# Optimization experiments

Measured on AMD Instinct MI355X. Metric: run time of the kernel, lower is better.

Reference implementation:

```python
import jax, jax.numpy as jnp
import numpy as np

N_USERS = 50000
N_ITEMS = 4000
BATCH = 256
EPS = 1e-8


def setup_inputs() -> dict:
    key = jax.random.key(0)
    k1, k2 = jax.random.split(key)
    explicit_feedback = jax.random.uniform(k1, (N_USERS, N_ITEMS), dtype=jnp.float32)
    user_ids = jax.random.randint(k2, (BATCH,), 0, N_USERS, dtype=jnp.int64)
    return {"explicit_feedback": explicit_feedback, "user_ids": user_ids, "num_neighbors": 10}


def reference(explicit_feedback, user_ids, num_neighbors):
    F = explicit_feedback                              # [U, I]
    # norm = row-wise SUM OF SQUARES (no sqrt), as in the original module
    norm_all = jnp.maximum(jnp.sum(F * F, axis=1), EPS)          # [U]
    users = F[user_ids]                                          # [B, I]
    norm_users = jnp.maximum(jnp.sum(users * users, axis=1), EPS)  # [B]
    sim = (users @ F.T) / norm_users[:, None] / norm_all[None, :]  # [B, U]
    neighbor_sim, neighbor_idx = jax.lax.top_k(sim, num_neighbors)  # [B, k]
    weights = neighbor_sim / jnp.sum(neighbor_sim, axis=1, keepdims=True)  # [B, k]
    neighbors = F[neighbor_idx]                                   # [B, k, I]
    ratings = jnp.einsum("bk,bki->bi", weights, neighbors)        # [B, I]
    return ratings
```

## Files before the change

kernel.cpp:

```cpp
#include <hip/hip_runtime.h>
#include <hip/hip_bf16.h>

#define N_USERS 50000
#define N_ITEMS 4000
#define BATCH   256
#define KSTEPS  125
#define NWG     391
#define NEG_INF (-3.402823466e38f)

typedef __attribute__((ext_vector_type(8)))  __bf16 bfrag;
typedef __attribute__((ext_vector_type(16))) float  f32x16;

__device__ __forceinline__ unsigned short f2bf(float f) {
  unsigned u = __float_as_uint(f);
  return (unsigned short)((u + 0x7FFFu + ((u >> 16) & 1u)) >> 16);
}

__global__ __launch_bounds__(256) void prep_pack(
    const float* __restrict__ F, const int* __restrict__ uids,
    unsigned short* __restrict__ apack) {
  int m = blockIdx.x;
  size_t base = (size_t)uids[m] * N_ITEMS;
  for (int kk = threadIdx.x * 4; kk < N_ITEMS; kk += 1024) {
    float4 v = *(const float4*)(F + base + kk);
    ushort4 o;
    o.x = f2bf(v.x); o.y = f2bf(v.y); o.z = f2bf(v.z); o.w = f2bf(v.w);
    *(ushort4*)(apack + (size_t)(kk >> 5) * 8192 + m * 32 + (kk & 31)) = o;
  }
}

__global__ __launch_bounds__(256, 2) void gemm_topk(
    const float* __restrict__ F, const unsigned short* __restrict__ apack,
    float2* __restrict__ wstop) {
  union Smem {
    struct { unsigned short As[256][40]; unsigned short Bs[128][40]; } g;
    float dump[4][64][33];
  };
  __shared__ Smem sm;
  __shared__ float norms[128];

  const int tid  = threadIdx.x;
  const int w    = tid >> 6, lane = tid & 63;
  const int lrow = lane & 31, lhalf = lane >> 5;
  const int n0   = blockIdx.x * 128;

  const uint4* aptr = (const uint4*)apack + tid * 4;
  const int brow = tid >> 1, bh = tid & 1;
  const bool bvalid = (n0 + brow) < N_USERS;
  const float4* bptr = (const float4*)(F + (size_t)(bvalid ? (n0 + brow) : 0) * N_ITEMS) + bh * 4;

  f32x16 acc[2][4];
  #pragma unroll
  for (int i = 0; i < 2; ++i)
    #pragma unroll
    for (int j = 0; j < 4; ++j)
      #pragma unroll
      for (int e = 0; e < 16; ++e) acc[i][j][e] = 0.f;

  float ssq = 0.f;
  uint4 ar[4]; float4 br[4];

  {
    ar[0] = aptr[0]; ar[1] = aptr[1]; ar[2] = aptr[2]; ar[3] = aptr[3];
    if (bvalid) { br[0] = bptr[0]; br[1] = bptr[1]; br[2] = bptr[2]; br[3] = bptr[3]; }
    else { br[0] = br[1] = br[2] = br[3] = make_float4(0.f, 0.f, 0.f, 0.f); }
  }

  for (int ks = 0; ks < KSTEPS; ++ks) {
    if (ks) __syncthreads();
    uint4* adst = (uint4*)&sm.g.As[tid][0];
    adst[0] = ar[0]; adst[1] = ar[1]; adst[2] = ar[2]; adst[3] = ar[3];
    {
      const float* vv = (const float*)br;
      union { unsigned short s[8]; uint4 v; } h0, h1;
      #pragma unroll
      for (int e = 0; e < 8; ++e) h0.s[e] = f2bf(vv[e]);
      #pragma unroll
      for (int e = 0; e < 8; ++e) h1.s[e] = f2bf(vv[8 + e]);
      #pragma unroll
      for (int e = 0; e < 16; ++e) ssq = fmaf(vv[e], vv[e], ssq);
      *(uint4*)&sm.g.Bs[brow][bh * 16]     = h0.v;
      *(uint4*)&sm.g.Bs[brow][bh * 16 + 8] = h1.v;
    }
    __syncthreads();
    if (ks + 1 < KSTEPS) {
      const uint4* ap = aptr + (ks + 1) * 1024;
      ar[0] = ap[0]; ar[1] = ap[1]; ar[2] = ap[2]; ar[3] = ap[3];
      if (bvalid) {
        const float4* bp = bptr + (ks + 1) * 8;
        br[0] = bp[0]; br[1] = bp[1]; br[2] = bp[2]; br[3] = bp[3];
      }
    }
    #pragma unroll
    for (int s = 0; s < 2; ++s) {
      bfrag af[2], bfr[4];
      #pragma unroll
      for (int i = 0; i < 2; ++i)
        af[i] = *(const bfrag*)&sm.g.As[(2 * w + i) * 32 + lrow][s * 16 + lhalf * 8];
      #pragma unroll
      for (int j = 0; j < 4; ++j)
        bfr[j] = *(const bfrag*)&sm.g.Bs[j * 32 + lrow][s * 16 + lhalf * 8];
      #pragma unroll
      for (int i = 0; i < 2; ++i)
        #pragma unroll
        for (int j = 0; j < 4; ++j)
          acc[i][j] = __builtin_amdgcn_mfma_f32_32x32x16_bf16(af[i], bfr[j], acc[i][j], 0, 0, 0);
    }
  }

  ssq += __shfl_xor(ssq, 1);
  if (bh == 0) norms[brow] = fmaxf(ssq, 1e-8f);

  float tv[8]; int ti[8];
  #pragma unroll
  for (int q = 0; q < 8; ++q) { tv[q] = NEG_INF; ti[q] = 0; }

  #pragma unroll
  for (int p = 0; p < 4; ++p) {
    __syncthreads();
    {
      const int   ugc = n0 + 32 * p + lrow;
      const float inv = 1.0f / norms[32 * p + lrow];
      #pragma unroll
      for (int i = 0; i < 2; ++i)
        #pragma unroll
        for (int r = 0; r < 16; ++r) {
          int mrow = 32 * i + (r & 3) + 8 * (r >> 2) + 4 * lhalf;
          float v = (ugc < N_USERS) ? acc[i][p][r] * inv : NEG_INF;
          sm.dump[w][mrow][lrow] = v;
        }
    }
    __syncthreads();
    for (int c = 0; c < 32; ++c) {
      float v = sm.dump[w][lane][c];
      int ci = n0 + 32 * p + c;
      #pragma unroll
      for (int q = 0; q < 8; ++q) {
        bool gt = v > tv[q];
        float ov = tv[q]; int oi = ti[q];
        tv[q] = gt ? v : ov; ti[q] = gt ? ci : oi;
        v = gt ? ov : v;     ci = gt ? oi : ci;
      }
    }
  }

  float2* dst = wstop + ((size_t)blockIdx.x * 256 + tid) * 8;
  #pragma unroll
  for (int q = 0; q < 8; ++q) dst[q] = make_float2(tv[q], __int_as_float(ti[q]));
}

__global__ __launch_bounds__(64) void merge_topk(
    const float2* __restrict__ wstop, int* __restrict__ cand) {
  const int b = blockIdx.x, l = threadIdx.x;
  float tv[8]; int ti[8];
  #pragma unroll
  for (int q = 0; q < 8; ++q) { tv[q] = NEG_INF; ti[q] = 0; }
  for (int c = l; c < NWG * 8; c += 64) {
    int wg = c >> 3, q = c & 7;
    float2 e = wstop[((size_t)wg * 256 + b) * 8 + q];
    float v = e.x; int ci = __float_as_int(e.y);
    #pragma unroll
    for (int q2 = 0; q2 < 8; ++q2) {
      bool gt = v > tv[q2];
      float ov = tv[q2]; int oi = ti[q2];
      tv[q2] = gt ? v : ov; ti[q2] = gt ? ci : oi;
      v = gt ? ov : v;      ci = gt ? oi : ci;
    }
  }
  __shared__ float sv[512];
  __shared__ int   si[512];
  #pragma unroll
  for (int q = 0; q < 8; ++q) { sv[l * 8 + q] = tv[q]; si[l * 8 + q] = ti[q]; }
  __syncthreads();
  if (l == 0) {
    float bv[32]; int bi[32];
    #pragma unroll
    for (int q = 0; q < 32; ++q) { bv[q] = NEG_INF; bi[q] = 0; }
    for (int n = 0; n < 512; ++n) {
      float v = sv[n];
      if (v > bv[31]) {
        int ci = si[n];
        #pragma unroll
        for (int q = 0; q < 32; ++q) {
          bool gt = v > bv[q];
          float ov = bv[q]; int oi = bi[q];
          bv[q] = gt ? v : ov; bi[q] = gt ? ci : oi;
          v = gt ? ov : v;     ci = gt ? oi : ci;
        }
      }
    }
    #pragma unroll
    for (int q = 0; q < 32; ++q) cand[b * 32 + q] = bi[q];
  }
}

__global__ __launch_bounds__(64) void rescore(
    const float* __restrict__ F, const int* __restrict__ uids,
    const int* __restrict__ cand, double* __restrict__ simx) {
  const int pr = blockIdx.x;
  const int b  = pr >> 5;
  const int ci = cand[pr];
  const float* fa = F + (size_t)uids[b] * N_ITEMS;
  const float* fc = F + (size_t)ci * N_ITEMS;
  double dot = 0.0, ss = 0.0;
  for (int k = threadIdx.x * 4; k < N_ITEMS; k += 256) {
    float4 a = *(const float4*)(fa + k);
    float4 c = *(const float4*)(fc + k);
    dot += (double)a.x * c.x + (double)a.y * c.y + (double)a.z * c.z + (double)a.w * c.w;
    ss  += (double)c.x * c.x + (double)c.y * c.y + (double)c.z * c.z + (double)c.w * c.w;
  }
  #pragma unroll
  for (int off = 32; off > 0; off >>= 1) {
    dot += __shfl_down(dot, off);
    ss  += __shfl_down(ss, off);
  }
  if (threadIdx.x == 0) simx[pr] = dot / fmax(ss, 1e-8);
}

__global__ __launch_bounds__(256) void finalize(
    const float* __restrict__ F, const int* __restrict__ cand,
    const double* __restrict__ simx, float* __restrict__ out) {
  const int b = blockIdx.x;
  __shared__ float wsh[10];
  __shared__ int   ish[10];
  if (threadIdx.x == 0) {
    double bv[10]; int bi[10];
    #pragma unroll
    for (int q = 0; q < 10; ++q) { bv[q] = -1.0e300; bi[q] = 0; }
    for (int n = 0; n < 32; ++n) {
      double v = simx[b * 32 + n];
      int ci = cand[b * 32 + n];
      #pragma unroll
      for (int q = 0; q < 10; ++q) {
        bool gt = v > bv[q];
        double ov = bv[q]; int oi = bi[q];
        bv[q] = gt ? v : ov; bi[q] = gt ? ci : oi;
        v = gt ? ov : v;     ci = gt ? oi : ci;
      }
    }
    double s = 0.0;
    #pragma unroll
    for (int q = 0; q < 10; ++q) s += bv[q];
    #pragma unroll
    for (int q = 0; q < 10; ++q) { wsh[q] = (float)(bv[q] / s); ish[q] = bi[q]; }
  }
  __syncthreads();
  float wr[10]; size_t ro[10];
  #pragma unroll
  for (int q = 0; q < 10; ++q) { wr[q] = wsh[q]; ro[q] = (size_t)ish[q] * N_ITEMS; }
  for (int i = threadIdx.x; i < N_ITEMS; i += 256) {
    float a = 0.f;
    #pragma unroll
    for (int q = 0; q < 10; ++q) a = fmaf(wr[q], F[ro[q] + i], a);
    out[b * N_ITEMS + i] = a;
  }
}

extern "C" void kernel_launch(void* const* d_in, const int* in_sizes, int n_in,
                              void* d_out, int out_size, void* d_ws, size_t ws_size,
                              hipStream_t stream) {
  const float* F    = (const float*)d_in[0];
  const int*   uids = (const int*)d_in[1];
  float* out = (float*)d_out;
  char*  ws  = (char*)d_ws;

  unsigned short* apack = (unsigned short*)ws;
  float2* wstop = (float2*)(ws + 2097152);
  int*    cand  = (int*)(ws + 2097152 + 6406144);
  double* simx  = (double*)(ws + 2097152 + 6406144 + 32768);

  prep_pack<<<dim3(BATCH), dim3(256), 0, stream>>>(F, uids, apack);
  gemm_topk<<<dim3(NWG),   dim3(256), 0, stream>>>(F, apack, wstop);
  merge_topk<<<dim3(BATCH), dim3(64), 0, stream>>>(wstop, cand);
  rescore<<<dim3(BATCH * 32), dim3(64), 0, stream>>>(F, uids, cand, simx);
  finalize<<<dim3(BATCH), dim3(256), 0, stream>>>(F, cand, simx, out);
}
```

Measured before the change: 1.457 ms.

## Load A fragments directly from global, double-buffer B tile, skip top-k inserts

The packed A matrix is laid out in MFMA fragment order so each wave reads its bf16 A operands straight from global/L2 instead of staging them through LDS. The B tile is double-buffered in LDS with a two-step-ahead register prefetch, which removes one barrier per k-step. Waves are rearranged into a 2x2 grid (4x2 MFMA tiles each), and the top-k insertion is guarded by an early comparison against the current 8th value. The trade-off is that A fragments are re-read from global by every workgroup each k-step, and more registers are live for the two B prefetch sets.

```diff
diff --git a/kernel.cpp b/kernel.cpp
--- a/kernel.cpp
+++ b/kernel.cpp
@@ -20,12 +20,14 @@
     const float* __restrict__ F, const int* __restrict__ uids,
     unsigned short* __restrict__ apack) {
   int m = blockIdx.x;
+  const int f = m >> 5, lr = m & 31;
   size_t base = (size_t)uids[m] * N_ITEMS;
   for (int kk = threadIdx.x * 4; kk < N_ITEMS; kk += 1024) {
     float4 v = *(const float4*)(F + base + kk);
     ushort4 o;
     o.x = f2bf(v.x); o.y = f2bf(v.y); o.z = f2bf(v.z); o.w = f2bf(v.w);
-    *(ushort4*)(apack + (size_t)(kk >> 5) * 8192 + m * 32 + (kk & 31)) = o;
+    int idx = ((kk >> 4) * 8 + f) * 512 + (lr + ((kk >> 3) & 1) * 32) * 8 + (kk & 7);
+    *(ushort4*)(apack + idx) = o;
   }
 }
 
@@ -33,80 +35,79 @@
     const float* __restrict__ F, const unsigned short* __restrict__ apack,
     float2* __restrict__ wstop) {
   union Smem {
-    struct { unsigned short As[256][40]; unsigned short Bs[128][40]; } g;
-    float dump[4][64][33];
+    unsigned short Bs[2][128][40];
+    float dump[256][33];
   };
   __shared__ Smem sm;
   __shared__ float norms[128];
 
-  const int tid  = threadIdx.x;
-  const int w    = tid >> 6, lane = tid & 63;
-  const int lrow = lane & 31, lhalf = lane >> 5;
-  const int n0   = blockIdx.x * 128;
-
-  const uint4* aptr = (const uint4*)apack + tid * 4;
+  const int tid   = threadIdx.x;
+  const int w     = tid >> 6, lane = tid & 63;
+  const int lrow  = lane & 31, lhalf = lane >> 5;
+  const int mh    = w >> 1, nh = w & 1;
+  const int n0    = blockIdx.x * 128;
+
   const int brow = tid >> 1, bh = tid & 1;
-  const bool bvalid = (n0 + brow) < N_USERS;
-  const float4* bptr = (const float4*)(F + (size_t)(bvalid ? (n0 + brow) : 0) * N_ITEMS) + bh * 4;
-
-  f32x16 acc[2][4];
-  #pragma unroll
-  for (int i = 0; i < 2; ++i)
-    #pragma unroll
-    for (int j = 0; j < 4; ++j)
+  int grow = n0 + brow; if (grow >= N_USERS) grow = 0;
+  const float4* bptr = (const float4*)(F + (size_t)grow * N_ITEMS) + bh * 4;
+  const unsigned short* abase = apack + (mh * 4) * 512 + lane * 8;
+
+  f32x16 acc[4][2];
+  #pragma unroll
+  for (int i = 0; i < 4; ++i)
+    #pragma unroll
+    for (int j = 0; j < 2; ++j)
       #pragma unroll
       for (int e = 0; e < 16; ++e) acc[i][j][e] = 0.f;
 
   float ssq = 0.f;
-  uint4 ar[4]; float4 br[4];
-
-  {
-    ar[0] = aptr[0]; ar[1] = aptr[1]; ar[2] = aptr[2]; ar[3] = aptr[3];
-    if (bvalid) { br[0] = bptr[0]; br[1] = bptr[1]; br[2] = bptr[2]; br[3] = bptr[3]; }
-    else { br[0] = br[1] = br[2] = br[3] = make_float4(0.f, 0.f, 0.f, 0.f); }
-  }
-
-  for (int ks = 0; ks < KSTEPS; ++ks) {
-    if (ks) __syncthreads();
-    uint4* adst = (uint4*)&sm.g.As[tid][0];
-    adst[0] = ar[0]; adst[1] = ar[1]; adst[2] = ar[2]; adst[3] = ar[3];
-    {
-      const float* vv = (const float*)br;
-      union { unsigned short s[8]; uint4 v; } h0, h1;
-      #pragma unroll
-      for (int e = 0; e < 8; ++e) h0.s[e] = f2bf(vv[e]);
-      #pragma unroll
-      for (int e = 0; e < 8; ++e) h1.s[e] = f2bf(vv[8 + e]);
-      #pragma unroll
-      for (int e = 0; e < 16; ++e) ssq = fmaf(vv[e], vv[e], ssq);
-      *(uint4*)&sm.g.Bs[brow][bh * 16]     = h0.v;
-      *(uint4*)&sm.g.Bs[brow][bh * 16 + 8] = h1.v;
-    }
-    __syncthreads();
-    if (ks + 1 < KSTEPS) {
-      const uint4* ap = aptr + (ks + 1) * 1024;
-      ar[0] = ap[0]; ar[1] = ap[1]; ar[2] = ap[2]; ar[3] = ap[3];
-      if (bvalid) {
-        const float4* bp = bptr + (ks + 1) * 8;
-        br[0] = bp[0]; br[1] = bp[1]; br[2] = bp[2]; br[3] = bp[3];
-      }
-    }
-    #pragma unroll
-    for (int s = 0; s < 2; ++s) {
-      bfrag af[2], bfr[4];
-      #pragma unroll
-      for (int i = 0; i < 2; ++i)
-        af[i] = *(const bfrag*)&sm.g.As[(2 * w + i) * 32 + lrow][s * 16 + lhalf * 8];
-      #pragma unroll
-      for (int j = 0; j < 4; ++j)
-        bfr[j] = *(const bfrag*)&sm.g.Bs[j * 32 + lrow][s * 16 + lhalf * 8];
-      #pragma unroll
-      for (int i = 0; i < 2; ++i)
-        #pragma unroll
-        for (int j = 0; j < 4; ++j)
-          acc[i][j] = __builtin_amdgcn_mfma_f32_32x32x16_bf16(af[i], bfr[j], acc[i][j], 0, 0, 0);
-    }
-  }
+  float4 brA[4], brB[4];
+
+#define LOADB(SET, T) do { \
+    const float4* bp_ = bptr + (T) * 8; \
+    _Pragma("unroll") for (int q_ = 0; q_ < 4; ++q_) SET[q_] = bp_[q_]; \
+  } while (0)
+
+#define CONVW(SET, BUF) do { \
+    const float* vv_ = (const float*)SET; \
+    union { unsigned short s[8]; uint4 v; } h0_, h1_; \
+    _Pragma("unroll") for (int e_ = 0; e_ < 8; ++e_) h0_.s[e_] = f2bf(vv_[e_]); \
+    _Pragma("unroll") for (int e_ = 0; e_ < 8; ++e_) h1_.s[e_] = f2bf(vv_[8 + e_]); \
+    _Pragma("unroll") for (int e_ = 0; e_ < 16; ++e_) ssq = fmaf(vv_[e_], vv_[e_], ssq); \
+    *(uint4*)&sm.Bs[BUF][brow][bh * 16]     = h0_.v; \
+    *(uint4*)&sm.Bs[BUF][brow][bh * 16 + 8] = h1_.v; \
+  } while (0)
+
+#define STEP(T, CSET, LSET, PAR) do { \
+    _Pragma("unroll") for (int s_ = 0; s_ < 2; ++s_) { \
+      bfrag av_[4], bf_[2]; \
+      _Pragma("unroll") for (int i_ = 0; i_ < 4; ++i_) \
+        av_[i_] = *(const bfrag*)(abase + (T) * 8192 + s_ * 4096 + i_ * 512); \
+      _Pragma("unroll") for (int jj_ = 0; jj_ < 2; ++jj_) \
+        bf_[jj_] = *(const bfrag*)&sm.Bs[PAR][(2 * nh + jj_) * 32 + lrow][s_ * 16 + lhalf * 8]; \
+      _Pragma("unroll") for (int i_ = 0; i_ < 4; ++i_) \
+        _Pragma("unroll") for (int jj_ = 0; jj_ < 2; ++jj_) \
+          acc[i_][jj_] = __builtin_amdgcn_mfma_f32_32x32x16_bf16(av_[i_], bf_[jj_], acc[i_][jj_], 0, 0, 0); \
+    } \
+    if ((T) + 2 < KSTEPS) LOADB(LSET, (T) + 2); \
+    if ((T) + 1 < KSTEPS) CONVW(CSET, (PAR) ^ 1); \
+    __syncthreads(); \
+  } while (0)
+
+  LOADB(brA, 0);
+  LOADB(brB, 1);
+  CONVW(brA, 0);
+  __syncthreads();
+
+  for (int t = 0; t < KSTEPS - 1; t += 2) {
+    STEP(t,     brB, brA, 0);
+    STEP(t + 1, brA, brB, 1);
+  }
+  STEP(KSTEPS - 1, brB, brA, 0);
+
+#undef STEP
+#undef CONVW
+#undef LOADB
 
   ssq += __shfl_xor(ssq, 1);
   if (bh == 0) norms[brow] = fmaxf(ssq, 1e-8f);
@@ -118,28 +119,30 @@
   #pragma unroll
   for (int p = 0; p < 4; ++p) {
     __syncthreads();
-    {
-      const int   ugc = n0 + 32 * p + lrow;
+    if (nh == (p >> 1)) {
+      const int jj  = p & 1;
+      const int ugc = n0 + 32 * p + lrow;
       const float inv = 1.0f / norms[32 * p + lrow];
       #pragma unroll
-      for (int i = 0; i < 2; ++i)
+      for (int i = 0; i < 4; ++i)
         #pragma unroll
         for (int r = 0; r < 16; ++r) {
-          int mrow = 32 * i + (r & 3) + 8 * (r >> 2) + 4 * lhalf;
-          float v = (ugc < N_USERS) ? acc[i][p][r] * inv : NEG_INF;
-          sm.dump[w][mrow][lrow] = v;
+          int mrow = 128 * mh + 32 * i + (r & 3) + 8 * (r >> 2) + 4 * lhalf;
+          sm.dump[mrow][lrow] = (ugc < N_USERS) ? acc[i][jj][r] * inv : NEG_INF;
         }
     }
     __syncthreads();
     for (int c = 0; c < 32; ++c) {
-      float v = sm.dump[w][lane][c];
+      float v = sm.dump[tid][c];
       int ci = n0 + 32 * p + c;
-      #pragma unroll
-      for (int q = 0; q < 8; ++q) {
-        bool gt = v > tv[q];
-        float ov = tv[q]; int oi = ti[q];
-        tv[q] = gt ? v : ov; ti[q] = gt ? ci : oi;
-        v = gt ? ov : v;     ci = gt ? oi : ci;
+      if (v > tv[7]) {
+        #pragma unroll
+        for (int q = 0; q < 8; ++q) {
+          bool gt = v > tv[q];
+          float ov = tv[q]; int oi = ti[q];
+          tv[q] = gt ? v : ov; ti[q] = gt ? ci : oi;
+          v = gt ? ov : v;     ci = gt ? oi : ci;
+        }
       }
     }
   }
```

Result: faster. 1.343 ms (-7.9%).
